# Optimization experiments

Hardware: AMD Instinct MI355X
Metric: run time of the kernel (lower is better)

Reference implementation:

```python
import jax, jax.numpy as jnp
import numpy as np

D_MODEL = 1024
NUM_HEADS = 16
OUT_SHAPE = (64,)            # ControlGate `shape`; d_head = prod(OUT_SHAPE)
BANK_SIZE = 16
TOP_K = 2
BATCH, SEQ = 8, 4096
D_OUT = NUM_HEADS * int(np.prod(OUT_SHAPE))  # 1024


def setup_inputs() -> dict:
    key = jax.random.key(0)
    k1, k2, k3, k4 = jax.random.split(key, 4)
    tensor = jax.random.normal(k1, (BATCH, SEQ, D_MODEL), dtype=jnp.float32)
    sel_idx = jax.random.randint(k2, (BATCH, TOP_K), 0, BANK_SIZE)
    sel_probs = jax.random.uniform(k3, (BATCH, TOP_K), dtype=jnp.float32)
    sel_probs = sel_probs / jnp.sum(sel_probs, axis=-1, keepdims=True)
    W = jax.random.normal(k4, (BANK_SIZE, D_MODEL, D_OUT), dtype=jnp.float32) * 0.02
    b = jnp.zeros((BANK_SIZE, D_OUT), dtype=jnp.float32)
    return {"tensor": tensor, "sel_idx": sel_idx, "sel_probs": sel_probs, "W": W, "b": b}


def reference(tensor, sel_idx, sel_probs, W, b):
    # --- VirtualMakeHeads: bank-selected (virtual) linear projection ---
    # Superimpose the selected weight banks per batch element.
    W_sel = W[sel_idx]                    # (B, K, d_model, d_out)  irregular gather
    b_sel = b[sel_idx]                    # (B, K, d_out)
    W_eff = jnp.einsum('bk,bkio->bio', sel_probs, W_sel)   # (B, d_model, d_out)
    b_eff = jnp.einsum('bk,bko->bo', sel_probs, b_sel)     # (B, d_out)
    logits = jnp.einsum('bsi,bio->bso', tensor, W_eff) + b_eff[:, None, :]
    # reshape to heads: (B, S, num_heads, d_head)
    logits = logits.reshape(*logits.shape[:-1], NUM_HEADS, -1)
    # --- ControlGate: unflatten last dim into OUT_SHAPE ---
    logits = logits.reshape(*logits.shape[:-1], *OUT_SHAPE)
    # DropoutLogits with p=0.0 (eval) is identity.
    # activation == 'sigmoid'
    return jax.nn.sigmoid(logits)
```

## Files before the change

### kernel.cpp

```cpp
#include <hip/hip_runtime.h>
#include <hip/hip_bf16.h>

#define B_  8
#define S_  4096
#define DM  1024
#define DO  1024

typedef __attribute__((ext_vector_type(4))) float f32x4;
typedef __attribute__((ext_vector_type(8))) short bf16x8;

__device__ inline unsigned int pkbf(float a, float b) {
    __hip_bfloat162 h = __float22bfloat162_rn(float2{a, b});
    union { __hip_bfloat162 h2; unsigned int u; } cv;
    cv.h2 = h;
    return cv.u;
}

__global__ __launch_bounds__(256) void prep_wpack(
    const float* __restrict__ W, const int* __restrict__ sel_idx,
    const float* __restrict__ sel_probs, unsigned short* __restrict__ wpack)
{
    const int kt = blockIdx.x, nb = blockIdx.y, b = blockIdx.z;
    const int i0 = sel_idx[b*2+0], i1 = sel_idx[b*2+1];
    const float p0 = sel_probs[b*2+0], p1 = sel_probs[b*2+1];
    const int col = threadIdx.x;
    const int half = col >> 7, colh = col & 127;

    const float* w0 = W + (size_t)i0 * DM * DO + (size_t)(kt * 64) * DO + nb * 256 + col;
    const float* w1 = W + (size_t)i1 * DM * DO + (size_t)(kt * 64) * DO + nb * 256 + col;

    char* dst = (char*)wpack + ((((size_t)b * 4 + nb) * 16 + kt) << 15)
              + half * 16384 + colh * 128;

    #pragma unroll
    for (int g = 0; g < 8; ++g) {
        float v[8];
        #pragma unroll
        for (int j = 0; j < 8; ++j)
            v[j] = p0 * w0[(size_t)(g * 8 + j) * DO] + p1 * w1[(size_t)(g * 8 + j) * DO];
        uint4 u;
        u.x = pkbf(v[0], v[1]); u.y = pkbf(v[2], v[3]);
        u.z = pkbf(v[4], v[5]); u.w = pkbf(v[6], v[7]);
        *reinterpret_cast<uint4*>(dst + ((g * 16) ^ ((colh & 7) << 4))) = u;
    }
}

__global__ __launch_bounds__(256) void prep_beff(
    const float* __restrict__ bias, const int* __restrict__ sel_idx,
    const float* __restrict__ sel_probs, float* __restrict__ beff)
{
    const int b = blockIdx.x;
    const int i0 = sel_idx[b*2+0], i1 = sel_idx[b*2+1];
    const float p0 = sel_probs[b*2+0], p1 = sel_probs[b*2+1];
    for (int o = threadIdx.x; o < DO; o += blockDim.x)
        beff[(size_t)b * DO + o] = p0 * bias[(size_t)i0 * DO + o]
                                 + p1 * bias[(size_t)i1 * DO + o];
}

__global__ __launch_bounds__(512, 1) void gemm8(
    const float* __restrict__ X, const unsigned short* __restrict__ wpack,
    const float* __restrict__ beff, float* __restrict__ out)
{
    extern __shared__ char lds[];

    const int id = blockIdx.x;
    const int swz = (id & 7) * 64 + (id >> 3);
    const int b  = swz >> 6;
    const int bm = (swz & 63) >> 2;
    const int nb = swz & 3;

    const int t = threadIdx.x;
    const int wave = t >> 6, lane = t & 63;
    const int wm = wave >> 2, wn = wave & 3;
    const int fr = lane & 15, fq = lane >> 4;

    const int s_row = t >> 3;
    const int s_g   = t & 7;
    const float* xbase = X + ((size_t)(b * S_ + bm * 256 + s_row)) * DM + s_g * 8;

    const unsigned short* wtile0 = wpack + (((size_t)b * 4 + nb) * 16) * 16384;

    const int swz0 = (fq * 16) ^ ((fr & 7) << 4);
    const int swz1 = (64 + fq * 16) ^ ((fr & 7) << 4);
    const int aTbase = wm * 16384 + fr * 128;
    const int bTbase = 32768 + (wn >> 1) * 16384 + ((wn & 1) * 64 + fr) * 128;

    f32x4 acc[8][4] = {};
    float4 ax[8];

    #pragma unroll
    for (int p = 0; p < 4; ++p) {
        ax[p * 2]     = *reinterpret_cast<const float4*>(xbase + (size_t)p * 64 * DM);
        ax[p * 2 + 1] = *reinterpret_cast<const float4*>(xbase + (size_t)p * 64 * DM + 4);
    }
    {
        const char* gB = (const char*)wtile0;
        #pragma unroll
        for (int i = 0; i < 4; ++i)
            __builtin_amdgcn_global_load_lds(
                (const __attribute__((address_space(1))) void*)(gB + wave * 4096 + i * 1024 + lane * 16),
                (__attribute__((address_space(3))) void*)(lds + 32768 + wave * 4096 + i * 1024),
                16, 0, 0);
    }
    #pragma unroll
    for (int p = 0; p < 4; ++p) {
        const int row = p * 64 + s_row;
        const int half = row >> 7, rowh = row & 127;
        uint4 u;
        u.x = pkbf(ax[p*2].x, ax[p*2].y);     u.y = pkbf(ax[p*2].z, ax[p*2].w);
        u.z = pkbf(ax[p*2+1].x, ax[p*2+1].y); u.w = pkbf(ax[p*2+1].z, ax[p*2+1].w);
        *reinterpret_cast<uint4*>(lds + half * 16384 + rowh * 128
                                  + ((s_g * 16) ^ ((rowh & 7) << 4))) = u;
    }
    __syncthreads();

    for (int kt = 0; kt < 16; ++kt) {
        char* bufc = lds + (kt & 1) * 65536;
        char* bufn = lds + ((kt + 1) & 1) * 65536;

        if (kt < 15) {
            #pragma unroll
            for (int p = 0; p < 4; ++p) {
                ax[p * 2]     = *reinterpret_cast<const float4*>(xbase + (size_t)p * 64 * DM + (kt + 1) * 64);
                ax[p * 2 + 1] = *reinterpret_cast<const float4*>(xbase + (size_t)p * 64 * DM + (kt + 1) * 64 + 4);
            }
            const char* gB = (const char*)(wtile0 + (size_t)(kt + 1) * 16384);
            #pragma unroll
            for (int i = 0; i < 4; ++i)
                __builtin_amdgcn_global_load_lds(
                    (const __attribute__((address_space(1))) void*)(gB + wave * 4096 + i * 1024 + lane * 16),
                    (__attribute__((address_space(3))) void*)(bufn + 32768 + wave * 4096 + i * 1024),
                    16, 0, 0);
        }

        bf16x8 bfrag[4][2];
        #pragma unroll
        for (int nf = 0; nf < 4; ++nf) {
            bfrag[nf][0] = *reinterpret_cast<const bf16x8*>(bufc + bTbase + nf * 2048 + swz0);
            bfrag[nf][1] = *reinterpret_cast<const bf16x8*>(bufc + bTbase + nf * 2048 + swz1);
        }

        #pragma unroll
        for (int p = 0; p < 4; ++p) {
            bf16x8 af[2][2];
            #pragma unroll
            for (int i = 0; i < 2; ++i) {
                af[i][0] = *reinterpret_cast<const bf16x8*>(bufc + aTbase + (2*p + i) * 2048 + swz0);
                af[i][1] = *reinterpret_cast<const bf16x8*>(bufc + aTbase + (2*p + i) * 2048 + swz1);
            }
            __builtin_amdgcn_s_barrier();
            __builtin_amdgcn_s_setprio(1);
            #pragma unroll
            for (int i = 0; i < 2; ++i) {
                #pragma unroll
                for (int nf = 0; nf < 4; ++nf) {
                    acc[2*p+i][nf] = __builtin_amdgcn_mfma_f32_16x16x32_bf16(af[i][0], bfrag[nf][0], acc[2*p+i][nf], 0, 0, 0);
                    acc[2*p+i][nf] = __builtin_amdgcn_mfma_f32_16x16x32_bf16(af[i][1], bfrag[nf][1], acc[2*p+i][nf], 0, 0, 0);
                }
            }
            __builtin_amdgcn_s_setprio(0);
            __builtin_amdgcn_s_barrier();
        }

        if (kt < 15) {
            #pragma unroll
            for (int p = 0; p < 4; ++p) {
                const int row = p * 64 + s_row;
                const int half = row >> 7, rowh = row & 127;
                uint4 u;
                u.x = pkbf(ax[p*2].x, ax[p*2].y);     u.y = pkbf(ax[p*2].z, ax[p*2].w);
                u.z = pkbf(ax[p*2+1].x, ax[p*2+1].y); u.w = pkbf(ax[p*2+1].z, ax[p*2+1].w);
                *reinterpret_cast<uint4*>(bufn + half * 16384 + rowh * 128
                                          + ((s_g * 16) ^ ((rowh & 7) << 4))) = u;
            }
        }
        __syncthreads();
    }

    const float* be = beff + (size_t)b * DO + nb * 256 + wn * 64;
    float bv[4];
    #pragma unroll
    for (int nf = 0; nf < 4; ++nf) bv[nf] = be[nf * 16 + fr];

    float* ob = out + ((size_t)(b * S_ + bm * 256 + wm * 128)) * DO + nb * 256 + wn * 64;
    #pragma unroll
    for (int mf = 0; mf < 8; ++mf) {
        #pragma unroll
        for (int nf = 0; nf < 4; ++nf) {
            const int col = nf * 16 + fr;
            #pragma unroll
            for (int r = 0; r < 4; ++r) {
                const int row = mf * 16 + fq * 4 + r;
                const float xv = acc[mf][nf][r] + bv[nf];
                ob[(size_t)row * DO + col] = 1.0f / (1.0f + __expf(-xv));
            }
        }
    }
}

extern "C" void kernel_launch(void* const* d_in, const int* in_sizes, int n_in,
                              void* d_out, int out_size, void* d_ws, size_t ws_size,
                              hipStream_t stream) {
    const float* tensor    = (const float*)d_in[0];
    const int*   sel_idx   = (const int*)d_in[1];
    const float* sel_probs = (const float*)d_in[2];
    const float* W         = (const float*)d_in[3];
    const float* bias      = (const float*)d_in[4];
    float* out = (float*)d_out;

    unsigned short* wpack = (unsigned short*)d_ws;
    float* beff = (float*)((char*)d_ws + (size_t)B_ * 4 * 16 * 32768);

    static bool attr_set = false;
    if (!attr_set) {
        hipFuncSetAttribute((const void*)gemm8,
                            hipFuncAttributeMaxDynamicSharedMemorySize, 131072);
        attr_set = true;
    }

    hipLaunchKernelGGL(prep_wpack, dim3(16, 4, 8), dim3(256), 0, stream,
                       W, sel_idx, sel_probs, wpack);
    hipLaunchKernelGGL(prep_beff, dim3(8), dim3(256), 0, stream,
                       bias, sel_idx, sel_probs, beff);
    hipLaunchKernelGGL(gemm8, dim3(512), dim3(512), 131072, stream,
                       tensor, wpack, beff, out);
}
```

Baseline: 163.8 us.

## Triple-buffer B tiles with prefetch distance two and split MFMA phases

Restructures the GEMM main loop so that weight tiles rotate through three LDS buffers and are prefetched two k-steps ahead with global_load_lds. The activation tile now uses a single LDS buffer. Explicit waitcnt and barriers replace __syncthreads. The inner compute is split into four phases, each loading one k-half of the A and B fragments, which shrinks the number of live fragment registers. The aim is to hide global-load latency for the weight tiles and to reduce register pressure. The cost is more barriers per step and a dependence on hand-placed waitcnt for correctness. The shared-memory attribute is now set on every launch.

```diff
diff --git a/kernel.cpp b/kernel.cpp
--- a/kernel.cpp
+++ b/kernel.cpp
@@ -77,104 +77,101 @@
     const int s_row = t >> 3;
     const int s_g   = t & 7;
     const float* xbase = X + ((size_t)(b * S_ + bm * 256 + s_row)) * DM + s_g * 8;
-
-    const unsigned short* wtile0 = wpack + (((size_t)b * 4 + nb) * 16) * 16384;
+    const char* wtile0 = (const char*)(wpack + (((size_t)b * 4 + nb) * 16) * 16384);
 
     const int swz0 = (fq * 16) ^ ((fr & 7) << 4);
     const int swz1 = (64 + fq * 16) ^ ((fr & 7) << 4);
-    const int aTbase = wm * 16384 + fr * 128;
-    const int bTbase = 32768 + (wn >> 1) * 16384 + ((wn & 1) * 64 + fr) * 128;
+    const int aTb = wm * 16384 + fr * 128;
+    const int bTb = (wn >> 1) * 16384 + ((wn & 1) * 64 + fr) * 128;
 
     f32x4 acc[8][4] = {};
     float4 ax[8];
 
-    #pragma unroll
-    for (int p = 0; p < 4; ++p) {
-        ax[p * 2]     = *reinterpret_cast<const float4*>(xbase + (size_t)p * 64 * DM);
-        ax[p * 2 + 1] = *reinterpret_cast<const float4*>(xbase + (size_t)p * 64 * DM + 4);
-    }
-    {
-        const char* gB = (const char*)wtile0;
-        #pragma unroll
-        for (int i = 0; i < 4; ++i)
-            __builtin_amdgcn_global_load_lds(
-                (const __attribute__((address_space(1))) void*)(gB + wave * 4096 + i * 1024 + lane * 16),
-                (__attribute__((address_space(3))) void*)(lds + 32768 + wave * 4096 + i * 1024),
-                16, 0, 0);
-    }
-    #pragma unroll
-    for (int p = 0; p < 4; ++p) {
-        const int row = p * 64 + s_row;
-        const int half = row >> 7, rowh = row & 127;
-        uint4 u;
-        u.x = pkbf(ax[p*2].x, ax[p*2].y);     u.y = pkbf(ax[p*2].z, ax[p*2].w);
-        u.z = pkbf(ax[p*2+1].x, ax[p*2+1].y); u.w = pkbf(ax[p*2+1].z, ax[p*2+1].w);
-        *reinterpret_cast<uint4*>(lds + half * 16384 + rowh * 128
-                                  + ((s_g * 16) ^ ((rowh & 7) << 4))) = u;
-    }
-    __syncthreads();
+#define LOAD_X(KT)                                                            \
+    _Pragma("unroll")                                                         \
+    for (int p = 0; p < 4; ++p) {                                             \
+        ax[p*2]   = *reinterpret_cast<const float4*>(xbase + (size_t)p*64*DM + (KT)*64);     \
+        ax[p*2+1] = *reinterpret_cast<const float4*>(xbase + (size_t)p*64*DM + (KT)*64 + 4); \
+    }
+
+#define STAGE_B(KT, BOFF)                                                     \
+    {                                                                         \
+        const char* gB = wtile0 + (size_t)(KT) * 32768;                       \
+        _Pragma("unroll")                                                     \
+        for (int i = 0; i < 4; ++i)                                           \
+            __builtin_amdgcn_global_load_lds(                                 \
+                (const __attribute__((address_space(1))) void*)(gB + wave*4096 + i*1024 + lane*16), \
+                (__attribute__((address_space(3))) void*)(lds + (BOFF) + wave*4096 + i*1024),       \
+                16, 0, 0);                                                    \
+    }
+
+#define WRITE_A()                                                             \
+    _Pragma("unroll")                                                         \
+    for (int p = 0; p < 4; ++p) {                                             \
+        const int row = p * 64 + s_row;                                       \
+        const int half = row >> 7, rowh = row & 127;                          \
+        uint4 u;                                                              \
+        u.x = pkbf(ax[p*2].x, ax[p*2].y);     u.y = pkbf(ax[p*2].z, ax[p*2].w);     \
+        u.z = pkbf(ax[p*2+1].x, ax[p*2+1].y); u.w = pkbf(ax[p*2+1].z, ax[p*2+1].w); \
+        *reinterpret_cast<uint4*>(lds + half*16384 + rowh*128                 \
+                                  + ((s_g*16) ^ ((rowh & 7) << 4))) = u;      \
+    }
+
+    LOAD_X(0);
+    __builtin_amdgcn_sched_barrier(0);
+    STAGE_B(0, 32768);
+    STAGE_B(1, 65536);
+    __builtin_amdgcn_sched_barrier(0);
+    WRITE_A();
+    asm volatile("s_waitcnt vmcnt(4) lgkmcnt(0)" ::: "memory");
+    __builtin_amdgcn_s_barrier();
+
+    int br = 32768, bmid = 65536, bw = 98304;
 
     for (int kt = 0; kt < 16; ++kt) {
-        char* bufc = lds + (kt & 1) * 65536;
-        char* bufn = lds + ((kt + 1) & 1) * 65536;
+        if (kt < 15) { LOAD_X(kt + 1); }
+        __builtin_amdgcn_sched_barrier(0);
+        if (kt < 14) { STAGE_B(kt + 2, bw); }
+        __builtin_amdgcn_sched_barrier(0);
+
+        const char* Bb = lds + br;
+        bf16x8 bks[4], af[4];
+
+#define PHASE(MFBASE, SK, RELOAD_B)                                           \
+        {                                                                     \
+            if (RELOAD_B) {                                                   \
+                _Pragma("unroll")                                             \
+                for (int nf = 0; nf < 4; ++nf)                                \
+                    bks[nf] = *reinterpret_cast<const bf16x8*>(Bb + bTb + nf*2048 + (SK)); \
+            }                                                                 \
+            _Pragma("unroll")                                                 \
+            for (int m = 0; m < 4; ++m)                                       \
+                af[m] = *reinterpret_cast<const bf16x8*>(lds + aTb + ((MFBASE)+m)*2048 + (SK)); \
+            __builtin_amdgcn_s_barrier();                                     \
+            __builtin_amdgcn_s_setprio(1);                                    \
+            _Pragma("unroll")                                                 \
+            for (int m = 0; m < 4; ++m) {                                     \
+                _Pragma("unroll")                                             \
+                for (int nf = 0; nf < 4; ++nf)                                \
+                    acc[(MFBASE)+m][nf] = __builtin_amdgcn_mfma_f32_16x16x32_bf16( \
+                        af[m], bks[nf], acc[(MFBASE)+m][nf], 0, 0, 0);        \
+            }                                                                 \
+            __builtin_amdgcn_s_setprio(0);                                    \
+            __builtin_amdgcn_s_barrier();                                     \
+        }
+
+        PHASE(0, swz0, 1)
+        PHASE(4, swz0, 0)
+        PHASE(0, swz1, 1)
+        PHASE(4, swz1, 0)
+#undef PHASE
 
         if (kt < 15) {
-            #pragma unroll
-            for (int p = 0; p < 4; ++p) {
-                ax[p * 2]     = *reinterpret_cast<const float4*>(xbase + (size_t)p * 64 * DM + (kt + 1) * 64);
-                ax[p * 2 + 1] = *reinterpret_cast<const float4*>(xbase + (size_t)p * 64 * DM + (kt + 1) * 64 + 4);
-            }
-            const char* gB = (const char*)(wtile0 + (size_t)(kt + 1) * 16384);
-            #pragma unroll
-            for (int i = 0; i < 4; ++i)
-                __builtin_amdgcn_global_load_lds(
-                    (const __attribute__((address_space(1))) void*)(gB + wave * 4096 + i * 1024 + lane * 16),
-                    (__attribute__((address_space(3))) void*)(bufn + 32768 + wave * 4096 + i * 1024),
-                    16, 0, 0);
-        }
-
-        bf16x8 bfrag[4][2];
-        #pragma unroll
-        for (int nf = 0; nf < 4; ++nf) {
-            bfrag[nf][0] = *reinterpret_cast<const bf16x8*>(bufc + bTbase + nf * 2048 + swz0);
-            bfrag[nf][1] = *reinterpret_cast<const bf16x8*>(bufc + bTbase + nf * 2048 + swz1);
-        }
-
-        #pragma unroll
-        for (int p = 0; p < 4; ++p) {
-            bf16x8 af[2][2];
-            #pragma unroll
-            for (int i = 0; i < 2; ++i) {
-                af[i][0] = *reinterpret_cast<const bf16x8*>(bufc + aTbase + (2*p + i) * 2048 + swz0);
-                af[i][1] = *reinterpret_cast<const bf16x8*>(bufc + aTbase + (2*p + i) * 2048 + swz1);
-            }
-            __builtin_amdgcn_s_barrier();
-            __builtin_amdgcn_s_setprio(1);
-            #pragma unroll
-            for (int i = 0; i < 2; ++i) {
-                #pragma unroll
-                for (int nf = 0; nf < 4; ++nf) {
-                    acc[2*p+i][nf] = __builtin_amdgcn_mfma_f32_16x16x32_bf16(af[i][0], bfrag[nf][0], acc[2*p+i][nf], 0, 0, 0);
-                    acc[2*p+i][nf] = __builtin_amdgcn_mfma_f32_16x16x32_bf16(af[i][1], bfrag[nf][1], acc[2*p+i][nf], 0, 0, 0);
-                }
-            }
-            __builtin_amdgcn_s_setprio(0);
+            WRITE_A();
+            asm volatile("s_waitcnt lgkmcnt(0)" ::: "memory");
             __builtin_amdgcn_s_barrier();
         }
-
-        if (kt < 15) {
-            #pragma unroll
-            for (int p = 0; p < 4; ++p) {
-                const int row = p * 64 + s_row;
-                const int half = row >> 7, rowh = row & 127;
-                uint4 u;
-                u.x = pkbf(ax[p*2].x, ax[p*2].y);     u.y = pkbf(ax[p*2].z, ax[p*2].w);
-                u.z = pkbf(ax[p*2+1].x, ax[p*2+1].y); u.w = pkbf(ax[p*2+1].z, ax[p*2+1].w);
-                *reinterpret_cast<uint4*>(bufn + half * 16384 + rowh * 128
-                                          + ((s_g * 16) ^ ((rowh & 7) << 4))) = u;
-            }
-        }
-        __syncthreads();
+        const int tmp = br; br = bmid; bmid = bw; bw = tmp;
     }
 
     const float* be = beff + (size_t)b * DO + nb * 256 + wn * 64;
@@ -196,6 +193,9 @@
             }
         }
     }
+#undef LOAD_X
+#undef STAGE_B
+#undef WRITE_A
 }
 
 extern "C" void kernel_launch(void* const* d_in, const int* in_sizes, int n_in,
@@ -211,12 +211,8 @@
     unsigned short* wpack = (unsigned short*)d_ws;
     float* beff = (float*)((char*)d_ws + (size_t)B_ * 4 * 16 * 32768);
 
-    static bool attr_set = false;
-    if (!attr_set) {
-        hipFuncSetAttribute((const void*)gemm8,
-                            hipFuncAttributeMaxDynamicSharedMemorySize, 131072);
-        attr_set = true;
-    }
+    hipFuncSetAttribute((const void*)gemm8,
+                        hipFuncAttributeMaxDynamicSharedMemorySize, 131072);
 
     hipLaunchKernelGGL(prep_wpack, dim3(16, 4, 8), dim3(256), 0, stream,
                        W, sel_idx, sel_probs, wpack);
```

Measured after the change: 143.0 us. 12.7% less time.
